# Performance work log

Hardware: AMD Instinct MI355X
Metric: run time of the kernel (lower is better)

## Reference

```python
import math
import jax, jax.numpy as jnp
import numpy as np

L, H = 4, 8  # num_layers, num_heads
SPARSE_FACTOR = 0.1
NEG = -1e9


def _ln(x, g, b, eps=1e-5):
    m = jnp.mean(x, axis=-1, keepdims=True)
    v = jnp.mean(jnp.square(x - m), axis=-1, keepdims=True)
    return (x - m) * jax.lax.rsqrt(v + eps) * g + b


def _pos_enc(S, D):
    # sinusoidal PE, shape (S, 1, D) matching pe.unsqueeze(0).transpose(0,1)[:S]
    pos = np.arange(S, dtype=np.float32)[:, None]
    div = np.exp(np.arange(0, D, 2, dtype=np.float32) * (-math.log(10000.0) / D))
    pe = np.zeros((S, D), dtype=np.float32)
    pe[:, 0::2] = np.sin(pos * div)
    pe[:, 1::2] = np.cos(pos * div)
    return jnp.asarray(pe)[:, None, :]


def setup_inputs() -> dict:
    key = jax.random.key(0)
    B, S, I, D, F = 128, 512, 64, 512, 2048
    ks = jax.random.split(key, 10)
    w = lambda k, shape: jax.random.normal(k, shape, jnp.float32) * 0.02
    return {
        'x': jax.random.normal(ks[0], (B, S, I), jnp.float32),
        'W_in': w(ks[1], (I, D)), 'b_in': jnp.zeros((D,), jnp.float32),
        'ln1_g': jnp.ones((L, D), jnp.float32), 'ln1_b': jnp.zeros((L, D), jnp.float32),
        'Wq': w(ks[2], (L, D, D)), 'Wk': w(ks[3], (L, D, D)), 'Wv': w(ks[4], (L, D, D)),
        'Wo': w(ks[5], (L, D, D)), 'bo': jnp.zeros((L, D), jnp.float32),
        'ln2_g': jnp.ones((L, D), jnp.float32), 'ln2_b': jnp.zeros((L, D), jnp.float32),
        'W1': w(ks[6], (L, D, F)), 'b1': jnp.zeros((L, F), jnp.float32),
        'W2': w(ks[7], (L, F, D)), 'b2': jnp.zeros((L, D), jnp.float32),
        'lnf_g': jnp.ones((D,), jnp.float32), 'lnf_b': jnp.zeros((D,), jnp.float32),
    }


def reference(x, W_in, b_in, ln1_g, ln1_b, Wq, Wk, Wv, Wo, bo,
              ln2_g, ln2_b, W1, b1, W2, b2, lnf_g, lnf_b):
    B, S, _ = x.shape
    D = W_in.shape[1]
    dk = D // H
    # source: scores last dim == batch (view+transpose quirk); k = max(1, int(B*0.1))
    topk = max(1, int(B * SPARSE_FACTOR))
    h = jnp.swapaxes(x, 0, 1) @ W_in + b_in          # (S,B,D)
    h = h * math.sqrt(D) + _pos_enc(S, D)

    def heads(z, w):
        return jnp.swapaxes((z @ w).reshape(S, B, H, dk), 1, 2)  # (S,H,B,dk)

    def body(h, p):
        g1, bb1, wq, wk, wv, wo, bo_, g2, bb2, w1, b1_, w2, b2_ = p
        y = _ln(h, g1, bb1)
        q, k, v = heads(y, wq), heads(y, wk), heads(y, wv)
        scores = jnp.einsum('shbd,shcd->shbc', q, k) / math.sqrt(dk)  # (S,H,B,B)
        kth = jax.lax.top_k(scores, topk)[0][..., -1:]
        scores = jnp.where(scores >= kth, scores, NEG)  # top-k sparsification
        attn = jax.nn.softmax(scores, axis=-1)
        ctx = jnp.einsum('shbc,shcd->shbd', attn, v)
        ctx = jnp.swapaxes(ctx, 1, 2).reshape(S, B, D)
        h = ctx @ wo + bo_ + h                       # attn out + residual
        f = jax.nn.gelu(_ln(h, g2, bb2) @ w1 + b1_, approximate=False) @ w2 + b2_
        return h + f, None

    h, _ = jax.lax.scan(body, h, (ln1_g, ln1_b, Wq, Wk, Wv, Wo, bo,
                                  ln2_g, ln2_b, W1, b1, W2, b2))
    h = _ln(h, lnf_g, lnf_b)
    return jnp.swapaxes(h, 0, 1)                     # (B,S,D)
```

## Files before the change

### kernel.cpp

```cpp
#include <hip/hip_runtime.h>
#include <math.h>

#define S_ 512
#define B_ 128
#define D_ 512
#define I_ 64
#define F_ 2048
#define H_ 8
#define DK_ 64
#define L_ 4
#define SB_ (S_*B_)

typedef unsigned short u16;
typedef unsigned int u32;
typedef __attribute__((ext_vector_type(4))) unsigned int u32x4;
typedef __attribute__((ext_vector_type(4))) float f32x4;

__device__ __forceinline__ u16 f2bf(float f){
  u32 x = __builtin_bit_cast(u32, f);
  x += 0x7fffu + ((x >> 16) & 1u);
  return (u16)(x >> 16);
}

__device__ __forceinline__ void mfma16(f32x4& c, const u32x4& a, const u32x4& b){
  asm volatile("v_mfma_f32_16x16x32_bf16 %0, %1, %2, %0" : "+v"(c) : "v"(a), "v"(b));
}

__device__ __forceinline__ void gload16(const u16* g, u16* l){
  __builtin_amdgcn_global_load_lds((const __attribute__((address_space(1))) unsigned int*)g,
                                   (__attribute__((address_space(3))) unsigned int*)l, 16, 0, 0);
}

__device__ __forceinline__ float gelu_fast(float x){
  float u = 0.7978845608028654f * fmaf(0.044715f*x*x, x, x);
  float ae = __expf(-2.f*fabsf(u));
  float th = (1.f - ae) / (1.f + ae);
  th = (u < 0.f) ? -th : th;
  return 0.5f * x * (1.f + th);
}

__global__ void pe_kernel(float* __restrict__ pe){
  int s = blockIdx.x, d = threadIdx.x;
  float e = expf((float)(d & ~1) * (-9.210340371976184f / (float)D_));
  float arg = (float)s * e;
  pe[s*D_ + d] = (d & 1) ? cosf(arg) : sinf(arg);
}

__global__ void transpose_bf16(const float* __restrict__ src, u16* __restrict__ dst,
                               int R, int C, size_t zstride){
  __shared__ float t[32][33];
  size_t sbase = (size_t)blockIdx.z * R * C;
  size_t dbase = (size_t)blockIdx.z * zstride;
  int r0 = blockIdx.y*32, c0 = blockIdx.x*32;
  int tx = threadIdx.x, ty = threadIdx.y;
  #pragma unroll
  for (int j=0;j<4;j++)
    t[ty+j*8][tx] = src[sbase + (size_t)(r0+ty+j*8)*C + c0+tx];
  __syncthreads();
  #pragma unroll
  for (int j=0;j<4;j++)
    dst[dbase + (size_t)(c0+ty+j*8)*R + r0+tx] = f2bf(t[tx][ty+j*8]);
}

__global__ __launch_bounds__(512) void inproj_kernel(const float* __restrict__ x,
    const float* __restrict__ Win, const float* __restrict__ bin,
    const float* __restrict__ pe, float* __restrict__ h){
  __shared__ float xs[8][64];
  int t = threadIdx.x;
  float w[64];
  #pragma unroll
  for (int i=0;i<64;i++) w[i] = Win[i*D_ + t];
  float bd = bin[t];
  int r0 = blockIdx.x * 128;
  for (int batch=0; batch<16; batch++){
    int rb = r0 + batch*8;
    {
      int rr = t >> 6, i = t & 63;
      int r = rb + rr;
      int s = r >> 7, b = r & 127;
      xs[rr][i] = x[((size_t)b*S_ + s)*I_ + i];
    }
    __syncthreads();
    float acc[8];
    #pragma unroll
    for (int rr=0;rr<8;rr++) acc[rr] = 0.f;
    #pragma unroll
    for (int i4=0;i4<16;i4++){
      f32x4 xv[8];
      #pragma unroll
      for (int rr=0;rr<8;rr++) xv[rr] = *(const f32x4*)&xs[rr][i4*4];
      #pragma unroll
      for (int rr=0;rr<8;rr++){
        acc[rr] = fmaf(xv[rr][0], w[i4*4+0], acc[rr]);
        acc[rr] = fmaf(xv[rr][1], w[i4*4+1], acc[rr]);
        acc[rr] = fmaf(xv[rr][2], w[i4*4+2], acc[rr]);
        acc[rr] = fmaf(xv[rr][3], w[i4*4+3], acc[rr]);
      }
    }
    #pragma unroll
    for (int rr=0;rr<8;rr++){
      int r = rb + rr;
      int s = r >> 7;
      h[(size_t)r*D_ + t] = (acc[rr] + bd) * 22.627416997969522f + pe[s*D_ + t];
    }
    __syncthreads();
  }
}

template<int FINAL>
__global__ __launch_bounds__(256) void ln_kernel(const float* __restrict__ hsrc,
    const float* __restrict__ g, const float* __restrict__ bb,
    u16* __restrict__ outb, float* __restrict__ outf){
  int row = blockIdx.x*4 + (threadIdx.x>>6);
  int lane = threadIdx.x & 63;
  const float* hr = hsrc + (size_t)row*D_ + lane*8;
  f32x4 a0 = *(const f32x4*)hr;
  f32x4 a1 = *(const f32x4*)(hr+4);
  float v[8];
  #pragma unroll
  for (int j=0;j<4;j++){ v[j]=a0[j]; v[4+j]=a1[j]; }
  float sum = 0.f;
  #pragma unroll
  for (int j=0;j<8;j++) sum += v[j];
  #pragma unroll
  for (int m=1;m<64;m<<=1) sum += __shfl_xor(sum, m);
  float mean = sum * (1.f/(float)D_);
  float s2 = 0.f;
  #pragma unroll
  for (int j=0;j<8;j++){ float dd = v[j]-mean; s2 = fmaf(dd,dd,s2); }
  #pragma unroll
  for (int m=1;m<64;m<<=1) s2 += __shfl_xor(s2, m);
  float inv = rsqrtf(s2*(1.f/(float)D_) + 1e-5f);
  f32x4 g0 = *(const f32x4*)&g[lane*8];
  f32x4 g1 = *(const f32x4*)&g[lane*8+4];
  f32x4 b0 = *(const f32x4*)&bb[lane*8];
  f32x4 b1 = *(const f32x4*)&bb[lane*8+4];
  float o[8];
  #pragma unroll
  for (int j=0;j<4;j++){
    o[j]   = (v[j]-mean)*inv*g0[j] + b0[j];
    o[4+j] = (v[4+j]-mean)*inv*g1[j] + b1[j];
  }
  if (FINAL == 0){
    u32x4 pk;
    #pragma unroll
    for (int j=0;j<4;j++)
      pk[j] = (u32)f2bf(o[2*j]) | ((u32)f2bf(o[2*j+1])<<16);
    *(u32x4*)&outb[(size_t)row*D_ + lane*8] = pk;
  } else {
    int s = row>>7, b = row&(B_-1);
    float* op = outf + ((size_t)b*S_ + s)*D_ + lane*8;
    f32x4 r0, r1;
    #pragma unroll
    for (int j=0;j<4;j++){ r0[j]=o[j]; r1[j]=o[4+j]; }
    *(f32x4*)op = r0;
    *(f32x4*)(op+4) = r1;
  }
}

template<int MODE>
__global__ __launch_bounds__(512) void gemm128(const u16* __restrict__ A,
    const u16* __restrict__ Wt, const float* __restrict__ bias,
    float* __restrict__ hres, u16* __restrict__ outb, int N, int K){
  const u32 nwg = gridDim.x * gridDim.y;
  u32 wg = blockIdx.y * gridDim.x + blockIdx.x;
  wg = (wg & 7) * (nwg >> 3) + (wg >> 3);
  const int m0 = (int)(wg / gridDim.x) * 128;
  const int n0 = (int)(wg % gridDim.x) * 256;
  __shared__ u16 a_lds[128*64];
  __shared__ u16 b_lds[256*64];
  const int t = threadIdx.x;
  const int lane = t & 63, wave = t >> 6;
  const int wm = wave >> 2, wn = wave & 3;
  const int rsel = lane & 15;
  const int kp0 = (((lane>>4)    ) ^ (rsel&7)) * 8;
  const int kp1 = (((lane>>4) | 4) ^ (rsel&7)) * 8;
  const int sl = (t&7) ^ ((t>>3)&7);
  const u16* ag = A  + (size_t)(m0 + (t>>3))*K + sl*8;
  const u16* bg = Wt + (size_t)(n0 + (t>>3))*K + sl*8;
  f32x4 acc[4][4] = {};
  for (int k0 = 0; k0 < K; k0 += 64){
    asm volatile("s_nop 7\n\ts_nop 7");
    __syncthreads();
    #pragma unroll
    for (int p=0;p<2;p++)
      gload16(ag + (size_t)(p*64)*K + k0, &a_lds[p*4096 + t*8]);
    #pragma unroll
    for (int p=0;p<4;p++)
      gload16(bg + (size_t)(p*64)*K + k0, &b_lds[p*4096 + t*8]);
    __syncthreads();
    u32x4 af[4], bfr[4];
    #pragma unroll
    for (int i=0;i<4;i++){
      af[i]  = *(const u32x4*)&a_lds[(wm*64 + i*16 + rsel)*64 + kp0];
      bfr[i] = *(const u32x4*)&b_lds[(wn*64 + i*16 + rsel)*64 + kp0];
    }
    #pragma unroll
    for (int i=0;i<4;i++)
      #pragma unroll
      for (int j=0;j<4;j++)
        mfma16(acc[i][j], af[i], bfr[j]);
    #pragma unroll
    for (int i=0;i<4;i++){
      af[i]  = *(const u32x4*)&a_lds[(wm*64 + i*16 + rsel)*64 + kp1];
      bfr[i] = *(const u32x4*)&b_lds[(wn*64 + i*16 + rsel)*64 + kp1];
    }
    #pragma unroll
    for (int i=0;i<4;i++)
      #pragma unroll
      for (int j=0;j<4;j++)
        mfma16(acc[i][j], af[i], bfr[j]);
  }
  asm volatile("s_nop 7\n\ts_nop 7");
  const int rb = (lane>>4)*4;
  #pragma unroll
  for (int i=0;i<4;i++){
    #pragma unroll
    for (int j=0;j<4;j++){
      int gn = n0 + wn*64 + j*16 + rsel;
      #pragma unroll
      for (int rg=0;rg<4;rg++){
        int gr = m0 + wm*64 + i*16 + rb + rg;
        float val = acc[i][j][rg];
        if (MODE == 0){
          int mat = gn >> 9;
          int hh = (gn >> 6) & 7, dd = gn & 63;
          int s = gr >> 7, b = gr & 127;
          u16* dst = outb + (size_t)mat*33554432ull;
          dst[(size_t)((s*H_ + hh)*B_ + b)*DK_ + dd] = f2bf(val);
        } else if (MODE == 1){
          hres[(size_t)gr*D_ + gn] += val + bias[gn];
        } else {
          outb[(size_t)gr*(size_t)N + gn] = f2bf(gelu_fast(val + bias[gn]));
        }
      }
    }
  }
}

__global__ __launch_bounds__(256, 2) void attn_kernel(const u16* __restrict__ qb,
    const u16* __restrict__ kb, const u16* __restrict__ vb, u16* __restrict__ cb){
  __shared__ __align__(16) char smem[80384];
  u16* q_lds = (u16*)smem;
  u16* k_lds = (u16*)(smem + 18432);
  float* S   = (float*)smem;
  u16* P     = (u16*)smem;
  u16* vT    = (u16*)(smem + 34816);
  u32* wl    = (u32*)(smem + 67584);
  float* rs  = (float*)(smem + 79872);
  int sh = blockIdx.x;
  int s = sh >> 3, hh = sh & 7;
  int t = threadIdx.x, lane = t & 63, wave = t >> 6;
  const u16* qg = qb + (size_t)sh * (B_*DK_);
  const u16* kg = kb + (size_t)sh * (B_*DK_);
  const u16* vg = vb + (size_t)sh * (B_*DK_);
  #pragma unroll
  for (int rr=0; rr<4; rr++){
    int idx = rr*2048 + t*8;
    int row = idx >> 6, col = idx & 63;
    *(u32x4*)&q_lds[row*72+col] = *(const u32x4*)&qg[idx];
    *(u32x4*)&k_lds[row*72+col] = *(const u32x4*)&kg[idx];
  }
  __syncthreads();
  int wm = wave>>1, wn = wave&1, rsel = lane & 15;
  f32x4 sacc[4][4] = {};
  #pragma unroll
  for (int ks=0; ks<2; ks++){
    asm volatile("s_nop 7\n\ts_nop 7");
    int ko = ks*32 + (lane>>4)*8;
    u32x4 qf[4], kf[4];
    #pragma unroll
    for (int i=0;i<4;i++){
      qf[i] = *(const u32x4*)&q_lds[(wm*64+i*16+rsel)*72 + ko];
      kf[i] = *(const u32x4*)&k_lds[(wn*64+i*16+rsel)*72 + ko];
    }
    #pragma unroll
    for (int i=0;i<4;i++)
      #pragma unroll
      for (int j=0;j<4;j++)
        mfma16(sacc[i][j], qf[i], kf[j]);
  }
  asm volatile("s_nop 7\n\ts_nop 7");
  __syncthreads();
  int rb = (lane>>4)*4;
  #pragma unroll
  for (int i=0;i<4;i++)
    #pragma unroll
    for (int j=0;j<4;j++)
      #pragma unroll
      for (int rg=0;rg<4;rg++)
        S[(wm*64+i*16+rb+rg)*132 + wn*64+j*16+rsel] = sacc[i][j][rg] * 0.125f;
  __syncthreads();
  int r = t >> 1, half = t & 1;
  const f32x4* srow4 = (const f32x4*)(S + r*132 + half*64);
  float kv[12];
  #pragma unroll
  for (int i=0;i<12;i++) kv[i] = -3.4e38f;
  for (int i4=0;i4<16;i4++){
    f32x4 v4 = srow4[i4];
    float m4 = fmaxf(fmaxf(v4[0],v4[1]), fmaxf(v4[2],v4[3]));
    if (m4 > kv[11]){
      #pragma unroll
      for (int z=0; z<4; z++){
        float inc = v4[z];
        if (inc > kv[11]){
          #pragma unroll
          for (int p=0;p<12;p++){
            float cur = kv[p];
            bool gt = inc > cur;
            kv[p] = gt ? inc : cur;
            inc   = gt ? cur : inc;
          }
        }
      }
    }
  }
  float kth = 3.4e38f;
  #pragma unroll
  for (int i=0;i<12;i++){
    float pb = __shfl_xor(kv[11-i], 1);
    kth = fminf(kth, fmaxf(kv[i], pb));
  }
  float mx = fmaxf(kv[0], __shfl_xor(kv[0], 1));
  float sum = 0.f;
  int n = 0;
  u32* myw = wl + t*12;
  for (int i4=0;i4<16;i4++){
    f32x4 v4 = srow4[i4];
    #pragma unroll
    for (int z=0; z<4; z++){
      float v = v4[z];
      if (v >= kth && n < 12){
        float e = __expf(v - mx);
        sum += e;
        myw[n] = ((u32)f2bf(e) << 16) | (u32)(half*64 + i4*4 + z);
        n++;
      }
    }
  }
  float tsum = sum + __shfl_xor(sum, 1);
  if (!half) rs[r] = 1.f / tsum;
  __syncthreads();
  {
    u32x4 zz = {0u,0u,0u,0u};
    #pragma unroll
    for (int z=0; z<9; z++){
      int idx = z*256 + t;
      if (idx < 2176) ((u32x4*)P)[idx] = zz;
    }
  }
  #pragma unroll
  for (int rr=0; rr<16; rr++){
    int idx2 = (rr*256 + t)*2;
    u32 u = *(const u32*)&vg[idx2];
    int c = idx2 >> 6, d0 = idx2 & 63;
    vT[d0*136 + c]     = (u16)(u & 0xffffu);
    vT[(d0+1)*136 + c] = (u16)(u >> 16);
  }
  __syncthreads();
  u16* prow = P + r*136;
  for (int j=0; j<n; j++){
    u32 e = myw[j];
    prow[e & 0xffffu] = (u16)(e >> 16);
  }
  __syncthreads();
  f32x4 cacc[4][2] = {};
  #pragma unroll
  for (int ks=0; ks<4; ks++){
    asm volatile("s_nop 7\n\ts_nop 7");
    int ko = ks*32 + (lane>>4)*8;
    u32x4 pf[4], vf[2];
    #pragma unroll
    for (int i=0;i<4;i++) pf[i] = *(const u32x4*)&P[(wm*64+i*16+rsel)*136 + ko];
    #pragma unroll
    for (int j=0;j<2;j++) vf[j] = *(const u32x4*)&vT[(wn*32+j*16+rsel)*136 + ko];
    #pragma unroll
    for (int i=0;i<4;i++)
      #pragma unroll
      for (int j=0;j<2;j++)
        mfma16(cacc[i][j], pf[i], vf[j]);
  }
  asm volatile("s_nop 7\n\ts_nop 7");
  #pragma unroll
  for (int i=0;i<4;i++)
    #pragma unroll
    for (int j=0;j<2;j++)
      #pragma unroll
      for (int rg=0;rg<4;rg++){
        int m = wm*64 + i*16 + rb + rg;
        int nn = wn*32 + j*16 + rsel;
        float val = cacc[i][j][rg] * rs[m];
        cb[((size_t)(s*B_ + m))*D_ + hh*DK_ + nn] = f2bf(val);
      }
}

extern "C" void kernel_launch(void* const* d_in, const int* in_sizes, int n_in,
                              void* d_out, int out_size, void* d_ws, size_t ws_size,
                              hipStream_t stream) {
  const float* x    = (const float*)d_in[0];
  const float* Win  = (const float*)d_in[1];
  const float* bin  = (const float*)d_in[2];
  const float* ln1g = (const float*)d_in[3];
  const float* ln1b = (const float*)d_in[4];
  const float* Wq   = (const float*)d_in[5];
  const float* Wk   = (const float*)d_in[6];
  const float* Wv   = (const float*)d_in[7];
  const float* Wo   = (const float*)d_in[8];
  const float* bo   = (const float*)d_in[9];
  const float* ln2g = (const float*)d_in[10];
  const float* ln2b = (const float*)d_in[11];
  const float* W1   = (const float*)d_in[12];
  const float* b1   = (const float*)d_in[13];
  const float* W2   = (const float*)d_in[14];
  const float* b2   = (const float*)d_in[15];
  const float* lnfg = (const float*)d_in[16];
  const float* lnfb = (const float*)d_in[17];

  char* ws = (char*)d_ws;
  float* h  = (float*)(ws);
  u16* yb   = (u16*)(ws + 134217728ull);
  u16* qb   = (u16*)(ws + 201326592ull);
  u16* kb   = (u16*)(ws + 268435456ull);
  u16* vb   = (u16*)(ws + 335544320ull);
  u16* cb   = (u16*)(ws + 402653184ull);
  u16* act  = qb;
  u16* wqkvT= (u16*)(ws + 469762048ull);
  u16* woT  = (u16*)(ws + 476053504ull);
  u16* w1T  = (u16*)(ws + 478150656ull);
  u16* w2T  = (u16*)(ws + 486539264ull);
  float* pe = (float*)(ws + 494927872ull);

  dim3 tb(32,8);
  pe_kernel<<<S_, D_, 0, stream>>>(pe);
  transpose_bf16<<<dim3(D_/32, D_/32, L_), tb, 0, stream>>>(Wq, wqkvT,            D_, D_, (size_t)3*D_*D_);
  transpose_bf16<<<dim3(D_/32, D_/32, L_), tb, 0, stream>>>(Wk, wqkvT + D_*D_,    D_, D_, (size_t)3*D_*D_);
  transpose_bf16<<<dim3(D_/32, D_/32, L_), tb, 0, stream>>>(Wv, wqkvT + 2*D_*D_,  D_, D_, (size_t)3*D_*D_);
  transpose_bf16<<<dim3(D_/32, D_/32, L_), tb, 0, stream>>>(Wo, woT,              D_, D_, (size_t)D_*D_);
  transpose_bf16<<<dim3(F_/32, D_/32, L_), tb, 0, stream>>>(W1, w1T, D_, F_, (size_t)D_*F_);
  transpose_bf16<<<dim3(D_/32, F_/32, L_), tb, 0, stream>>>(W2, w2T, F_, D_, (size_t)F_*D_);
  inproj_kernel<<<512, 512, 0, stream>>>(x, Win, bin, pe, h);

  ln_kernel<0><<<SB_/4, 256, 0, stream>>>(h, ln1g, ln1b, yb, nullptr);
  for (int l=0; l<L_; l++){
    gemm128<0><<<dim3(6,512), 512, 0, stream>>>(yb, wqkvT + (size_t)l*3*D_*D_, nullptr, nullptr, qb, 1536, D_);
    attn_kernel<<<S_*H_, 256, 0, stream>>>(qb, kb, vb, cb);
    gemm128<1><<<dim3(2,512), 512, 0, stream>>>(cb, woT + (size_t)l*D_*D_, bo + l*D_, h, nullptr, D_, D_);
    ln_kernel<0><<<SB_/4, 256, 0, stream>>>(h, ln2g + l*D_, ln2b + l*D_, yb, nullptr);
    gemm128<2><<<dim3(8,512), 512, 0, stream>>>(yb, w1T + (size_t)l*D_*F_, b1 + l*F_, nullptr, act, F_, D_);
    gemm128<1><<<dim3(2,512), 512, 0, stream>>>(act, w2T + (size_t)l*F_*D_, b2 + l*D_, h, nullptr, D_, F_);
    if (l < L_-1)
      ln_kernel<0><<<SB_/4, 256, 0, stream>>>(h, ln1g + (l+1)*D_, ln1b + (l+1)*D_, yb, nullptr);
  }
  ln_kernel<1><<<SB_/4, 256, 0, stream>>>(h, lnfg, lnfb, nullptr, (float*)d_out);
}
```

Before: 3.445 ms.

## Add 128x128 four-wave GEMM for FFN1 and prefetch V in attention

```diff
diff --git a/kernel.cpp b/kernel.cpp
--- a/kernel.cpp
+++ b/kernel.cpp
@@ -159,7 +159,7 @@
 }
 
 template<int MODE>
-__global__ __launch_bounds__(512) void gemm128(const u16* __restrict__ A,
+__global__ __launch_bounds__(512) void gemm256n(const u16* __restrict__ A,
     const u16* __restrict__ Wt, const float* __restrict__ bias,
     float* __restrict__ hres, u16* __restrict__ outb, int N, int K){
   const u32 nwg = gridDim.x * gridDim.y;
@@ -238,6 +238,85 @@
   }
 }
 
+template<int MODE>
+__global__ __launch_bounds__(256) void gemm4w(const u16* __restrict__ A,
+    const u16* __restrict__ Wt, const float* __restrict__ bias,
+    float* __restrict__ hres, u16* __restrict__ outb, int N, int K){
+  const u32 nwg = gridDim.x * gridDim.y;
+  u32 wg = blockIdx.y * gridDim.x + blockIdx.x;
+  wg = (wg & 7) * (nwg >> 3) + (wg >> 3);
+  const int m0 = (int)(wg / gridDim.x) * 128;
+  const int n0 = (int)(wg % gridDim.x) * 128;
+  __shared__ u16 a_lds[128*64];
+  __shared__ u16 b_lds[128*64];
+  const int t = threadIdx.x;
+  const int lane = t & 63, wave = t >> 6;
+  const int wm = wave >> 1, wn = wave & 1;
+  const int rsel = lane & 15;
+  const int kp0 = (((lane>>4)    ) ^ (rsel&7)) * 8;
+  const int kp1 = (((lane>>4) | 4) ^ (rsel&7)) * 8;
+  const int sl = (t&7) ^ ((t>>3)&7);
+  const u16* ag = A  + (size_t)(m0 + (t>>3))*K + sl*8;
+  const u16* bg = Wt + (size_t)(n0 + (t>>3))*K + sl*8;
+  f32x4 acc[4][4] = {};
+  for (int k0 = 0; k0 < K; k0 += 64){
+    asm volatile("s_nop 7\n\ts_nop 7");
+    __syncthreads();
+    #pragma unroll
+    for (int p=0;p<4;p++){
+      gload16(ag + (size_t)(p*32)*K + k0, &a_lds[p*2048 + t*8]);
+      gload16(bg + (size_t)(p*32)*K + k0, &b_lds[p*2048 + t*8]);
+    }
+    __syncthreads();
+    u32x4 af[4], bfr[4];
+    #pragma unroll
+    for (int i=0;i<4;i++){
+      af[i]  = *(const u32x4*)&a_lds[(wm*64 + i*16 + rsel)*64 + kp0];
+      bfr[i] = *(const u32x4*)&b_lds[(wn*64 + i*16 + rsel)*64 + kp0];
+    }
+    #pragma unroll
+    for (int i=0;i<4;i++)
+      #pragma unroll
+      for (int j=0;j<4;j++)
+        mfma16(acc[i][j], af[i], bfr[j]);
+    #pragma unroll
+    for (int i=0;i<4;i++){
+      af[i]  = *(const u32x4*)&a_lds[(wm*64 + i*16 + rsel)*64 + kp1];
+      bfr[i] = *(const u32x4*)&b_lds[(wn*64 + i*16 + rsel)*64 + kp1];
+    }
+    #pragma unroll
+    for (int i=0;i<4;i++)
+      #pragma unroll
+      for (int j=0;j<4;j++)
+        mfma16(acc[i][j], af[i], bfr[j]);
+  }
+  asm volatile("s_nop 7\n\ts_nop 7");
+  const int rb = (lane>>4)*4;
+  #pragma unroll
+  for (int i=0;i<4;i++){
+    #pragma unroll
+    for (int j=0;j<4;j++){
+      int gn = n0 + wn*64 + j*16 + rsel;
+      #pragma unroll
+      for (int rg=0;rg<4;rg++){
+        int gr = m0 + wm*64 + i*16 + rb + rg;
+        float val = acc[i][j][rg];
+        if (MODE == 0){
+          int mat = gn >> 9;
+          int hh = (gn >> 6) & 7, dd = gn & 63;
+          int s = gr >> 7, b = gr & 127;
+          u16* dst = outb + (size_t)mat*33554432ull;
+          dst[(size_t)((s*H_ + hh)*B_ + b)*DK_ + dd] = f2bf(val);
+        } else if (MODE == 1){
+          hres[(size_t)gr*D_ + gn] += val + bias[gn];
+        } else {
+          outb[(size_t)gr*(size_t)N + gn] = f2bf(gelu_fast(val + bias[gn]));
+        }
+      }
+    }
+  }
+}
+
 __global__ __launch_bounds__(256, 2) void attn_kernel(const u16* __restrict__ qb,
     const u16* __restrict__ kb, const u16* __restrict__ vb, u16* __restrict__ cb){
   __shared__ __align__(16) char smem[80384];
@@ -254,6 +333,10 @@
   const u16* qg = qb + (size_t)sh * (B_*DK_);
   const u16* kg = kb + (size_t)sh * (B_*DK_);
   const u16* vg = vb + (size_t)sh * (B_*DK_);
+  u32x4 vr0 = *(const u32x4*)&vg[t*32];
+  u32x4 vr1 = *(const u32x4*)&vg[t*32 + 8];
+  u32x4 vr2 = *(const u32x4*)&vg[t*32 + 16];
+  u32x4 vr3 = *(const u32x4*)&vg[t*32 + 24];
   #pragma unroll
   for (int rr=0; rr<4; rr++){
     int idx = rr*2048 + t*8;
@@ -343,25 +426,29 @@
   __syncthreads();
   {
     u32x4 zz = {0u,0u,0u,0u};
-    #pragma unroll
-    for (int z=0; z<9; z++){
-      int idx = z*256 + t;
-      if (idx < 2176) ((u32x4*)P)[idx] = zz;
-    }
-  }
-  #pragma unroll
-  for (int rr=0; rr<16; rr++){
-    int idx2 = (rr*256 + t)*2;
-    u32 u = *(const u32*)&vg[idx2];
-    int c = idx2 >> 6, d0 = idx2 & 63;
-    vT[d0*136 + c]     = (u16)(u & 0xffffu);
-    vT[(d0+1)*136 + c] = (u16)(u >> 16);
-  }
-  __syncthreads();
+    u16* pz = P + r*136 + half*64;
+    #pragma unroll
+    for (int z=0; z<8; z++) ((u32x4*)pz)[z] = zz;
+  }
   u16* prow = P + r*136;
   for (int j=0; j<n; j++){
     u32 e = myw[j];
     prow[e & 0xffffu] = (u16)(e >> 16);
+  }
+  #pragma unroll
+  for (int q4=0; q4<4; q4++){
+    u32 u0 = (q4==0?vr0[0]:q4==1?vr1[0]:q4==2?vr2[0]:vr3[0]);
+    u32 u1 = (q4==0?vr0[1]:q4==1?vr1[1]:q4==2?vr2[1]:vr3[1]);
+    u32 u2 = (q4==0?vr0[2]:q4==1?vr1[2]:q4==2?vr2[2]:vr3[2]);
+    u32 u3 = (q4==0?vr0[3]:q4==1?vr1[3]:q4==2?vr2[3]:vr3[3]);
+    u32 uu[4] = {u0,u1,u2,u3};
+    #pragma unroll
+    for (int z=0; z<4; z++){
+      int idx2 = t*32 + q4*8 + z*2;
+      int c = idx2 >> 6, d0 = idx2 & 63;
+      vT[d0*136 + c]     = (u16)(uu[z] & 0xffffu);
+      vT[(d0+1)*136 + c] = (u16)(uu[z] >> 16);
+    }
   }
   __syncthreads();
   f32x4 cacc[4][2] = {};
@@ -442,12 +529,12 @@
 
   ln_kernel<0><<<SB_/4, 256, 0, stream>>>(h, ln1g, ln1b, yb, nullptr);
   for (int l=0; l<L_; l++){
-    gemm128<0><<<dim3(6,512), 512, 0, stream>>>(yb, wqkvT + (size_t)l*3*D_*D_, nullptr, nullptr, qb, 1536, D_);
+    gemm256n<0><<<dim3(6,512), 512, 0, stream>>>(yb, wqkvT + (size_t)l*3*D_*D_, nullptr, nullptr, qb, 1536, D_);
     attn_kernel<<<S_*H_, 256, 0, stream>>>(qb, kb, vb, cb);
-    gemm128<1><<<dim3(2,512), 512, 0, stream>>>(cb, woT + (size_t)l*D_*D_, bo + l*D_, h, nullptr, D_, D_);
+    gemm256n<1><<<dim3(2,512), 512, 0, stream>>>(cb, woT + (size_t)l*D_*D_, bo + l*D_, h, nullptr, D_, D_);
     ln_kernel<0><<<SB_/4, 256, 0, stream>>>(h, ln2g + l*D_, ln2b + l*D_, yb, nullptr);
-    gemm128<2><<<dim3(8,512), 512, 0, stream>>>(yb, w1T + (size_t)l*D_*F_, b1 + l*F_, nullptr, act, F_, D_);
-    gemm128<1><<<dim3(2,512), 512, 0, stream>>>(act, w2T + (size_t)l*F_*D_, b2 + l*D_, h, nullptr, D_, F_);
+    gemm4w<2><<<dim3(16,512), 256, 0, stream>>>(yb, w1T + (size_t)l*D_*F_, b1 + l*F_, nullptr, act, F_, D_);
+    gemm256n<1><<<dim3(2,512), 512, 0, stream>>>(act, w2T + (size_t)l*F_*D_, b2 + l*D_, h, nullptr, D_, F_);
     if (l < L_-1)
       ln_kernel<0><<<SB_/4, 256, 0, stream>>>(h, ln1g + (l+1)*D_, ln1b + (l+1)*D_, yb, nullptr);
   }
```

After: 3.424 ms, median of 3. No clear change (-0.6%).
